# Kernel tuning notes

Hardware: AMD Instinct MI355X
Metric: run time of the kernel (lower is better)

## Reference

```python
import jax, jax.numpy as jnp
import numpy as np

N, E = 50000, 800000
CUR, HID, OUT = 128, 96, 128
NEG_SLOPE = 0.01  # F.leaky_relu default


def setup_inputs() -> dict:
    key = jax.random.key(0)
    ks = jax.random.split(key, 12)
    inv = lambda d: 1.0 / np.sqrt(d)
    return {
        "h": jax.random.normal(ks[0], (N, CUR), jnp.float32),
        "x": jax.random.normal(ks[1], (N, CUR), jnp.float32),
        "edge_index": jax.random.randint(ks[2], (2, E), 0, N, dtype=jnp.int64),
        "edge_weight": jax.random.uniform(ks[3], (E,), jnp.float32),
        # preprocessor_x: Linear(cur_dim, hidden_dim)
        "pre_W": jax.random.uniform(ks[4], (CUR, HID), jnp.float32, -inv(CUR), inv(CUR)),
        "pre_b": jax.random.uniform(ks[5], (HID,), jnp.float32, -inv(CUR), inv(CUR)),
        # SAGEConv(hidden, out): lin_l (neighbor, with bias) + lin_r (root, no bias)
        "sage_Wl": jax.random.uniform(ks[6], (HID, OUT), jnp.float32, -inv(HID), inv(HID)),
        "sage_bl": jnp.zeros((OUT,), jnp.float32),
        "sage_Wr": jax.random.uniform(ks[7], (HID, OUT), jnp.float32, -inv(HID), inv(HID)),
        # ARMAConv(hidden, out) with K=1 stacks, T=1 layers (PyG defaults)
        "arma_W": jax.random.uniform(ks[8], (HID, OUT), jnp.float32, -inv(HID), inv(HID)),
        "arma_V": jax.random.uniform(ks[9], (HID, OUT), jnp.float32, -inv(HID), inv(HID)),
        "arma_b": jnp.zeros((OUT,), jnp.float32),
    }


def _cell(x, src, dst, edge_weight, pre_W, pre_b,
          sage_Wl, sage_bl, sage_Wr, arma_W, arma_V, arma_b):
    n = x.shape[0]
    xh = x @ pre_W + pre_b  # [N, HID]

    # ---- SAGEConv: mean aggregation of edge-weighted neighbor features ----
    msg = xh[src] * edge_weight[:, None]                     # [E, HID]
    aggr = jax.ops.segment_sum(msg, dst, num_segments=n)     # [N, HID]
    cnt = jax.ops.segment_sum(jnp.ones_like(edge_weight), dst, num_segments=n)
    mean = aggr / jnp.maximum(cnt, 1.0)[:, None]
    o_sage = mean @ sage_Wl + sage_bl + xh @ sage_Wr         # [N, OUT]

    # ---- ARMAConv (K=1, T=1): ReLU(L_hat (x W) + x V + b) ----
    deg = jax.ops.segment_sum(edge_weight, dst, num_segments=n)
    dinv = jnp.where(deg > 0, jax.lax.rsqrt(jnp.maximum(deg, 1e-30)), 0.0)
    norm = dinv[src] * edge_weight * dinv[dst]               # [E]
    xw = xh @ arma_W                                         # [N, OUT]
    prop = jax.ops.segment_sum(xw[src] * norm[:, None], dst, num_segments=n)
    o_arma = jax.nn.relu(prop + xh @ arma_V + arma_b)        # [N, OUT]

    o1 = jax.nn.leaky_relu(o_sage, NEG_SLOPE)
    o2 = jax.nn.leaky_relu(o_arma, NEG_SLOPE)
    return jax.nn.relu(o1 + o2)


def reference(h, x, edge_index, edge_weight, pre_W, pre_b,
              sage_Wl, sage_bl, sage_Wr, arma_W, arma_V, arma_b):
    src, dst = edge_index[0], edge_index[1]
    his = x
    o3 = _cell(x, src, dst, edge_weight, pre_W, pre_b,
               sage_Wl, sage_bl, sage_Wr, arma_W, arma_V, arma_b)
    return (his, o3)
```

## Files before the change

kernel.cpp:

```cpp
#include <hip/hip_runtime.h>


typedef __attribute__((ext_vector_type(8))) short bf16x8;
typedef __attribute__((ext_vector_type(4))) float f32x4;

__device__ __forceinline__ float bf2f(unsigned short u) {
    return __uint_as_float(((unsigned)u) << 16);
}
__device__ __forceinline__ unsigned short f2bf(float f) {
    unsigned u = __float_as_uint(f);
    return (unsigned short)((u + 0x7FFFu + ((u >> 16) & 1u)) >> 16);
}

__device__ __forceinline__ int edge_src(const int* ei, int e, int E, int flag) {
    return flag ? ei[2 * e] : ei[e];
}
__device__ __forceinline__ int edge_dst(const int* ei, int e, int E, int flag) {
    return flag ? ei[2 * (E + e)] : ei[E + e];
}

__global__ void k_wprep(const unsigned* __restrict__ eiu,
                        const float* __restrict__ Wl, const float* __restrict__ Wr,
                        const float* __restrict__ Wa, const float* __restrict__ Va,
                        const float* __restrict__ preW,
                        unsigned short* __restrict__ Wf_s,
                        unsigned short* __restrict__ Wf_a,
                        unsigned short* __restrict__ Wfp,
                        int* __restrict__ flag,
                        int4* __restrict__ cnt4, int nz4) {
    if (blockIdx.x == 0) {
        __shared__ int bad;
        if (threadIdx.x == 0) bad = 0;
        __syncthreads();
        int nb = 0;
#pragma unroll
        for (int q = 0; q < 4; q++) {
            unsigned w = eiu[2 * (threadIdx.x * 4 + q) + 1];
            if (w != 0) nb++;
        }
        if (nb) atomicAdd(&bad, nb);
        __syncthreads();
        if (threadIdx.x == 0) *flag = (bad == 0) ? 1 : 0;
        return;
    }
    int tid = (blockIdx.x - 1) * blockDim.x + threadIdx.x;
    if (tid < 6144) {
        int mat = tid / 3072, rem = tid % 3072;
        int kstep = rem / 512, rem2 = rem % 512;
        int g = rem2 / 128, j = rem2 % 128;
        int k0 = kstep * 32 + g * 8;
        const float* Wtop = mat ? Wa : Wl;
        const float* Wbot = mat ? Va : Wr;
        unsigned short* dst = (mat ? Wf_a : Wf_s) + (((size_t)(kstep * 4 + g) * 128 + j) * 8);
#pragma unroll
        for (int kk = 0; kk < 8; kk++) {
            int k = k0 + kk;
            float v = (k < 96) ? Wtop[k * 128 + j] : Wbot[(k - 96) * 128 + j];
            dst[kk] = f2bf(v);
        }
    } else if (tid < 7680) {
        int rem = tid - 6144;
        int kstep = rem / 384, rem2 = rem % 384;
        int g = rem2 / 96, j = rem2 % 96;
        int k0 = kstep * 32 + g * 8;
        unsigned short* dst = Wfp + (((size_t)(kstep * 4 + g) * 96 + j) * 8);
#pragma unroll
        for (int kk = 0; kk < 8; kk++) dst[kk] = f2bf(preW[(k0 + kk) * 96 + j]);
    } else if (tid >= 8192 && tid < 8192 + nz4) {
        cnt4[tid - 8192] = make_int4(0, 0, 0, 0);
    }
}

__global__ __launch_bounds__(256) void k_xh_count(
    const float* __restrict__ x, const unsigned short* __restrict__ Wfp,
    const float* __restrict__ b, unsigned short* __restrict__ xhbf,
    float* __restrict__ out0, int N, int xhBlocks,
    const int* __restrict__ ei, int* __restrict__ cntS, int* __restrict__ pos,
    int E, const int* __restrict__ flagp) {
    __shared__ unsigned short X[64][136];
    if (blockIdx.x >= xhBlocks) {
        int e = (blockIdx.x - xhBlocks) * 256 + threadIdx.x;
        if (e < E) {
            int flag = *flagp;
            int d = edge_dst(ei, e, E, flag);
            int shard = blockIdx.x & 7;
            int lp = atomicAdd(&cntS[(size_t)shard * N + d], 1);
            pos[e] = (lp << 3) | shard;
        }
        return;
    }
    int t = threadIdx.x;
    int nb = blockIdx.x * 64;
    for (int u = t; u < 2048; u += 256) {
        int row = u >> 5, q = u & 31;
        long gn = nb + row;
        float4 v = make_float4(0.f, 0.f, 0.f, 0.f);
        if (gn < N) {
            v = ((const float4*)(x + gn * 128))[q];
            ((float4*)(out0 + gn * 128))[q] = v;
        }
        unsigned short* p = &X[row][q * 4];
        p[0] = f2bf(v.x); p[1] = f2bf(v.y); p[2] = f2bf(v.z); p[3] = f2bf(v.w);
    }
    __syncthreads();
    int lane = t & 63, w = t >> 6;
    int lr = lane & 15, lg = lane >> 4;
    bf16x8 a[4];
#pragma unroll
    for (int ks = 0; ks < 4; ks++)
        a[ks] = *(const bf16x8*)&X[w * 16 + lr][ks * 32 + lg * 8];
    for (int jt = 0; jt < 6; jt++) {
        f32x4 acc = {0.f, 0.f, 0.f, 0.f};
#pragma unroll
        for (int ks = 0; ks < 4; ks++) {
            bf16x8 bf = *(const bf16x8*)(Wfp + (((size_t)(ks * 4 + lg) * 96 + jt * 16 + lr) * 8));
            acc = __builtin_amdgcn_mfma_f32_16x16x32_bf16(a[ks], bf, acc, 0, 0, 0);
        }
        int h = jt * 16 + lr;
        float bb = b[h];
#pragma unroll
        for (int r = 0; r < 4; r++) {
            long n = nb + w * 16 + lg * 4 + r;
            if (n < N) xhbf[n * 96 + h] = f2bf(acc[r] + bb);
        }
    }
}

__global__ void k_scan_blk(const int* __restrict__ cntS, int* __restrict__ sdelta,
                           int* __restrict__ offs, int* __restrict__ bsum, int N) {
    __shared__ int sh[256];
    int t = threadIdx.x;
    int n = blockIdx.x * 256 + t;
    int total = 0;
    if (n < N) {
        int run = 0;
#pragma unroll
        for (int s = 0; s < 8; s++) {
            sdelta[(size_t)s * N + n] = run;
            run += cntS[(size_t)s * N + n];
        }
        total = run;
    }
    sh[t] = total;
    __syncthreads();
    for (int off = 1; off < 256; off <<= 1) {
        int add = (t >= off) ? sh[t - off] : 0;
        __syncthreads();
        sh[t] += add;
        __syncthreads();
    }
    if (n < N) offs[n + 1] = sh[t];
    if (t == 255) bsum[blockIdx.x] = sh[255];
    if (blockIdx.x == 0 && t == 0) offs[0] = 0;
}

__global__ void k_scan_top(int* __restrict__ bsum, int nb) {
    __shared__ int sh[256];
    int t = threadIdx.x;
    sh[t] = (t < nb) ? bsum[t] : 0;
    __syncthreads();
    for (int off = 1; off < 256; off <<= 1) {
        int add = (t >= off) ? sh[t - off] : 0;
        __syncthreads();
        sh[t] += add;
        __syncthreads();
    }
    bsum[t] = sh[t];
}

__global__ void k_scan_add(int* __restrict__ offs, const int* __restrict__ bsum, int N) {
    int t = threadIdx.x;
    int n = blockIdx.x * 256 + t;
    if (n < N && blockIdx.x > 0) offs[n + 1] += bsum[blockIdx.x - 1];
}

__global__ void k_fill(const int* __restrict__ ei, const float* __restrict__ ew,
                       const int* __restrict__ offs, const int* __restrict__ sdelta,
                       const int* __restrict__ pos, int* __restrict__ esrc,
                       float* __restrict__ eww, int E, int N,
                       const int* __restrict__ flagp) {
    int e = blockIdx.x * blockDim.x + threadIdx.x;
    if (e >= E) return;
    int flag = *flagp;
    int s = edge_src(ei, e, E, flag);
    int d = edge_dst(ei, e, E, flag);
    int pp = pos[e];
    int shard = pp & 7, lp = pp >> 3;
    int idx = offs[d] + sdelta[(size_t)shard * N + d] + lp;
    esrc[idx] = s;
    eww[idx] = ew[e];
}

__global__ void k_degcsr(const float* __restrict__ eww, const int* __restrict__ offs,
                         float* __restrict__ dinv, float* __restrict__ minv, int N) {
    int n = blockIdx.x * blockDim.x + threadIdx.x;
    if (n >= N) return;
    int beg = offs[n], end = offs[n + 1];
    float dg = 0.f;
    for (int e = beg; e < end; e++) dg += eww[e];
    dinv[n] = dg > 0.f ? rsqrtf(fmaxf(dg, 1e-30f)) : 0.f;
    minv[n] = 1.f / fmaxf((float)(end - beg), 1.f);
}

__global__ __launch_bounds__(256) void k_gather(
    const int* __restrict__ esrc, const float* __restrict__ eww,
    const unsigned short* __restrict__ xhbf, const int* __restrict__ offs,
    const float* __restrict__ dinv, const float* __restrict__ minv,
    unsigned short* __restrict__ meanbf, unsigned short* __restrict__ propbf, int N) {
    int lane = threadIdx.x & 63;
    int d = __builtin_amdgcn_readfirstlane(blockIdx.x * 4 + (threadIdx.x >> 6));
    if (d >= N) return;
    int beg = offs[d], end = offs[d + 1];
    bool act = lane < 48;
    int col = 2 * lane;
    float s0 = 0.f, s1 = 0.f, a0 = 0.f, a1 = 0.f;
    int e = beg;
    for (; e + 8 <= end; e += 8) {
        int idx[8]; float wgt[8], dv[8]; unsigned v[8];
#pragma unroll
        for (int q = 0; q < 8; q++) { idx[q] = esrc[e + q]; wgt[q] = eww[e + q]; }
#pragma unroll
        for (int q = 0; q < 8; q++) dv[q] = dinv[idx[q]];
#pragma unroll
        for (int q = 0; q < 8; q++)
            v[q] = act ? *(const unsigned*)(xhbf + (size_t)idx[q] * 96 + col) : 0u;
#pragma unroll
        for (int q = 0; q < 8; q++) {
            float x0 = bf2f((unsigned short)(v[q] & 0xffff));
            float x1 = bf2f((unsigned short)(v[q] >> 16));
            float w2 = wgt[q], dw = dv[q] * w2;
            s0 += w2 * x0; s1 += w2 * x1;
            a0 += dw * x0; a1 += dw * x1;
        }
    }
    for (; e + 4 <= end; e += 4) {
        int idx[4]; float wgt[4], dv[4]; unsigned v[4];
#pragma unroll
        for (int q = 0; q < 4; q++) { idx[q] = esrc[e + q]; wgt[q] = eww[e + q]; }
#pragma unroll
        for (int q = 0; q < 4; q++) dv[q] = dinv[idx[q]];
#pragma unroll
        for (int q = 0; q < 4; q++)
            v[q] = act ? *(const unsigned*)(xhbf + (size_t)idx[q] * 96 + col) : 0u;
#pragma unroll
        for (int q = 0; q < 4; q++) {
            float x0 = bf2f((unsigned short)(v[q] & 0xffff));
            float x1 = bf2f((unsigned short)(v[q] >> 16));
            float w2 = wgt[q], dw = dv[q] * w2;
            s0 += w2 * x0; s1 += w2 * x1;
            a0 += dw * x0; a1 += dw * x1;
        }
    }
    for (; e < end; e++) {
        int s = esrc[e];
        float w2 = eww[e];
        float ds = dinv[s];
        if (act) {
            unsigned v = *(const unsigned*)(xhbf + (size_t)s * 96 + col);
            float x0 = bf2f((unsigned short)(v & 0xffff));
            float x1 = bf2f((unsigned short)(v >> 16));
            s0 += w2 * x0; s1 += w2 * x1;
            a0 += ds * w2 * x0; a1 += ds * w2 * x1;
        }
    }
    if (act) {
        float mi = minv[d], di = dinv[d];
        unsigned mo = (unsigned)f2bf(s0 * mi) | ((unsigned)f2bf(s1 * mi) << 16);
        unsigned po = (unsigned)f2bf(a0 * di) | ((unsigned)f2bf(a1 * di) << 16);
        *(unsigned*)(meanbf + (size_t)d * 96 + col) = mo;
        *(unsigned*)(propbf + (size_t)d * 96 + col) = po;
    }
}

__global__ __launch_bounds__(256) void k_out(
    const unsigned short* __restrict__ meanbf, const unsigned short* __restrict__ propbf,
    const unsigned short* __restrict__ xhbf, const unsigned short* __restrict__ Wf_s,
    const unsigned short* __restrict__ Wf_a, const float* __restrict__ bl,
    const float* __restrict__ ba, float* __restrict__ out, int N) {
    __shared__ unsigned short A[3][64][104];
    int t = threadIdx.x;
    int nb = blockIdx.x * 64;
    for (int u = t; u < 2304; u += 256) {
        int arr = u / 768, rem = u - arr * 768;
        int row = rem / 12, c = rem - row * 12;
        long gn = nb + row;
        const unsigned short* src = (arr == 0) ? meanbf : (arr == 1) ? propbf : xhbf;
        float4 v = (gn < N) ? *(const float4*)(src + gn * 96 + c * 8)
                            : make_float4(0.f, 0.f, 0.f, 0.f);
        *(float4*)&A[arr][row][c * 8] = v;
    }
    __syncthreads();
    int lane = t & 63, w = t >> 6;
    int lr = lane & 15, lg = lane >> 4;
    bf16x8 am[3], ap[3], ax[3];
#pragma unroll
    for (int ks = 0; ks < 3; ks++) {
        int row = w * 16 + lr, kc = ks * 32 + lg * 8;
        am[ks] = *(const bf16x8*)&A[0][row][kc];
        ap[ks] = *(const bf16x8*)&A[1][row][kc];
        ax[ks] = *(const bf16x8*)&A[2][row][kc];
    }
    for (int jt = 0; jt < 8; jt++) {
        f32x4 accS = {0.f, 0.f, 0.f, 0.f};
        f32x4 accA = {0.f, 0.f, 0.f, 0.f};
#pragma unroll
        for (int ks = 0; ks < 3; ks++) {
            size_t boffS = ((size_t)(ks * 4 + lg) * 128 + jt * 16 + lr) * 8;
            size_t boffS2 = ((size_t)((ks + 3) * 4 + lg) * 128 + jt * 16 + lr) * 8;
            bf16x8 b0 = *(const bf16x8*)(Wf_s + boffS);
            bf16x8 b1 = *(const bf16x8*)(Wf_s + boffS2);
            bf16x8 b2 = *(const bf16x8*)(Wf_a + boffS);
            bf16x8 b3 = *(const bf16x8*)(Wf_a + boffS2);
            accS = __builtin_amdgcn_mfma_f32_16x16x32_bf16(am[ks], b0, accS, 0, 0, 0);
            accS = __builtin_amdgcn_mfma_f32_16x16x32_bf16(ax[ks], b1, accS, 0, 0, 0);
            accA = __builtin_amdgcn_mfma_f32_16x16x32_bf16(ap[ks], b2, accA, 0, 0, 0);
            accA = __builtin_amdgcn_mfma_f32_16x16x32_bf16(ax[ks], b3, accA, 0, 0, 0);
        }
        int j = jt * 16 + lr;
        float blj = bl[j], baj = ba[j];
#pragma unroll
        for (int r = 0; r < 4; r++) {
            long n = nb + w * 16 + lg * 4 + r;
            if (n < N) {
                float os = accS[r] + blj;
                float oa = fmaxf(accA[r] + baj, 0.f);
                float o1 = os > 0.f ? os : 0.01f * os;
                float o2 = oa > 0.f ? oa : 0.01f * oa;
                out[n * 128 + j] = fmaxf(o1 + o2, 0.f);
            }
        }
    }
}

extern "C" void kernel_launch(void* const* d_in, const int* in_sizes, int n_in,
                              void* d_out, int out_size, void* d_ws, size_t ws_size,
                              hipStream_t stream) {
    const float* x    = (const float*)d_in[1];
    const int*   ei   = (const int*)d_in[2];
    const float* ew   = (const float*)d_in[3];
    const float* preW = (const float*)d_in[4];
    const float* preb = (const float*)d_in[5];
    const float* Wl   = (const float*)d_in[6];
    const float* bl   = (const float*)d_in[7];
    const float* Wr   = (const float*)d_in[8];
    const float* Wa   = (const float*)d_in[9];
    const float* Va   = (const float*)d_in[10];
    const float* ba   = (const float*)d_in[11];

    const int N = in_sizes[1] / 128;
    const int E = in_sizes[3];
    const int NB = (N + 255) / 256;

    char* w = (char*)d_ws;
    unsigned short* xhbf   = (unsigned short*)w; w += (size_t)N * 96 * 2;
    unsigned short* meanbf = (unsigned short*)w; w += (size_t)N * 96 * 2;
    unsigned short* propbf = (unsigned short*)w; w += (size_t)N * 96 * 2;
    unsigned short* Wf_s   = (unsigned short*)w; w += (size_t)6 * 4 * 128 * 8 * 2;
    unsigned short* Wf_a   = (unsigned short*)w; w += (size_t)6 * 4 * 128 * 8 * 2;
    unsigned short* Wfp    = (unsigned short*)w; w += (size_t)4 * 4 * 96 * 8 * 2;
    int*   esrc   = (int*)w;   w += (size_t)E * 4;
    float* eww    = (float*)w; w += (size_t)E * 4;
    int*   pos    = (int*)w;   w += (size_t)E * 4;
    int*   cntS   = (int*)w;   w += (size_t)8 * N * 4;
    int*   sdelta = (int*)w;   w += (size_t)8 * N * 4;
    float* dinv   = (float*)w; w += (size_t)N * 4;
    float* minv   = (float*)w; w += (size_t)N * 4;
    int*   offs   = (int*)w;   w += (size_t)(N + 1) * 4;
    int*   bsum   = (int*)w;   w += 256 * 4;
    int*   flag   = (int*)w;

    const int nz4 = (8 * N + 3) / 4;
    const int wprep_blocks = 1 + (8192 + nz4 + 255) / 256;
    const int xhBlocks = (N + 63) / 64;
    const int cntBlocks = (E + 255) / 256;

    k_wprep<<<wprep_blocks, 256, 0, stream>>>((const unsigned*)ei, Wl, Wr, Wa, Va,
                                              preW, Wf_s, Wf_a, Wfp, flag,
                                              (int4*)cntS, nz4);
    k_xh_count<<<xhBlocks + cntBlocks, 256, 0, stream>>>(
        x, Wfp, preb, xhbf, (float*)d_out, N, xhBlocks, ei, cntS, pos, E, flag);
    k_scan_blk<<<NB, 256, 0, stream>>>(cntS, sdelta, offs, bsum, N);
    k_scan_top<<<1, 256, 0, stream>>>(bsum, NB);
    k_scan_add<<<NB, 256, 0, stream>>>(offs, bsum, N);
    k_fill<<<(E + 255) / 256, 256, 0, stream>>>(ei, ew, offs, sdelta, pos, esrc,
                                                eww, E, N, flag);
    k_degcsr<<<NB, 256, 0, stream>>>(eww, offs, dinv, minv, N);
    k_gather<<<(N + 3) / 4, 256, 0, stream>>>(esrc, eww, xhbf, offs, dinv,
                                              minv, meanbf, propbf, N);
    k_out<<<(N + 63) / 64, 256, 0, stream>>>(meanbf, propbf, xhbf, Wf_s, Wf_a,
                                             bl, ba, (float*)d_out + (size_t)N * 128, N);
}
```

Before: 147.5 us.

## Fuse scan, fill and degree kernels into one persistent kernel with grid barriers

Merges the three-stage block scan, CSR fill and degree computation into a single kernel of NB (~196) blocks, separated by software grid barriers built on atomic counters placed right after cntS so the existing zeroing covers them. This removes four kernel launches and their inter-kernel gaps. The cost is spin-wait barriers, which depend on all blocks being co-resident, and a fill phase that now runs on far fewer threads (each block loops over a slice of edges).

```diff
diff --git a/kernel.cpp b/kernel.cpp
--- a/kernel.cpp
+++ b/kernel.cpp
@@ -17,6 +17,17 @@
 }
 __device__ __forceinline__ int edge_dst(const int* ei, int e, int E, int flag) {
     return flag ? ei[2 * (E + e)] : ei[E + e];
+}
+
+__device__ __forceinline__ void gbar(int* ctr, int nb) {
+    __syncthreads();
+    if (threadIdx.x == 0) {
+        __threadfence();
+        atomicAdd(ctr, 1);
+        while (__hip_atomic_load(ctr, __ATOMIC_RELAXED, __HIP_MEMORY_SCOPE_AGENT) < nb) {}
+    }
+    __syncthreads();
+    __threadfence();
 }
 
 __global__ void k_wprep(const unsigned* __restrict__ eiu,
@@ -126,10 +137,16 @@
     }
 }
 
-__global__ void k_scan_blk(const int* __restrict__ cntS, int* __restrict__ sdelta,
-                           int* __restrict__ offs, int* __restrict__ bsum, int N) {
+__global__ __launch_bounds__(256) void k_mid(
+    const int* __restrict__ ei, const float* __restrict__ ew,
+    int* __restrict__ cntS, int* __restrict__ sdelta, int* __restrict__ offs,
+    int* __restrict__ bsum, int* __restrict__ bars,
+    const int* __restrict__ pos, int* __restrict__ esrc, float* __restrict__ eww,
+    float* __restrict__ dinv, float* __restrict__ minv,
+    int E, int N, int eperblk, const int* __restrict__ flagp) {
     __shared__ int sh[256];
     int t = threadIdx.x;
+    int nb_ = gridDim.x;
     int n = blockIdx.x * 256 + t;
     int total = 0;
     if (n < N) {
@@ -149,57 +166,41 @@
         sh[t] += add;
         __syncthreads();
     }
-    if (n < N) offs[n + 1] = sh[t];
+    int local_incl = sh[t];
     if (t == 255) bsum[blockIdx.x] = sh[255];
     if (blockIdx.x == 0 && t == 0) offs[0] = 0;
-}
-
-__global__ void k_scan_top(int* __restrict__ bsum, int nb) {
-    __shared__ int sh[256];
-    int t = threadIdx.x;
-    sh[t] = (t < nb) ? bsum[t] : 0;
-    __syncthreads();
-    for (int off = 1; off < 256; off <<= 1) {
-        int add = (t >= off) ? sh[t - off] : 0;
-        __syncthreads();
-        sh[t] += add;
-        __syncthreads();
-    }
-    bsum[t] = sh[t];
-}
-
-__global__ void k_scan_add(int* __restrict__ offs, const int* __restrict__ bsum, int N) {
-    int t = threadIdx.x;
-    int n = blockIdx.x * 256 + t;
-    if (n < N && blockIdx.x > 0) offs[n + 1] += bsum[blockIdx.x - 1];
-}
-
-__global__ void k_fill(const int* __restrict__ ei, const float* __restrict__ ew,
-                       const int* __restrict__ offs, const int* __restrict__ sdelta,
-                       const int* __restrict__ pos, int* __restrict__ esrc,
-                       float* __restrict__ eww, int E, int N,
-                       const int* __restrict__ flagp) {
-    int e = blockIdx.x * blockDim.x + threadIdx.x;
-    if (e >= E) return;
-    int flag = *flagp;
-    int s = edge_src(ei, e, E, flag);
-    int d = edge_dst(ei, e, E, flag);
-    int pp = pos[e];
-    int shard = pp & 7, lp = pp >> 3;
-    int idx = offs[d] + sdelta[(size_t)shard * N + d] + lp;
-    esrc[idx] = s;
-    eww[idx] = ew[e];
-}
-
-__global__ void k_degcsr(const float* __restrict__ eww, const int* __restrict__ offs,
-                         float* __restrict__ dinv, float* __restrict__ minv, int N) {
-    int n = blockIdx.x * blockDim.x + threadIdx.x;
-    if (n >= N) return;
-    int beg = offs[n], end = offs[n + 1];
-    float dg = 0.f;
-    for (int e = beg; e < end; e++) dg += eww[e];
-    dinv[n] = dg > 0.f ? rsqrtf(fmaxf(dg, 1e-30f)) : 0.f;
-    minv[n] = 1.f / fmaxf((float)(end - beg), 1.f);
+    gbar(&bars[0], nb_);
+    sh[t] = (t < blockIdx.x) ? bsum[t] : 0;
+    __syncthreads();
+    for (int s = 128; s > 0; s >>= 1) {
+        if (t < s) sh[t] += sh[t + s];
+        __syncthreads();
+    }
+    int base = sh[0];
+    if (n < N) offs[n + 1] = base + local_incl;
+    gbar(&bars[1], nb_);
+    {
+        int flag = *flagp;
+        int e0 = blockIdx.x * eperblk;
+        int e1 = min(e0 + eperblk, E);
+        for (int e = e0 + t; e < e1; e += 256) {
+            int s = edge_src(ei, e, E, flag);
+            int d = edge_dst(ei, e, E, flag);
+            int pp = pos[e];
+            int shard = pp & 7, lp = pp >> 3;
+            int idx = offs[d] + sdelta[(size_t)shard * N + d] + lp;
+            esrc[idx] = s;
+            eww[idx] = ew[e];
+        }
+    }
+    gbar(&bars[2], nb_);
+    if (n < N) {
+        int beg = offs[n], end = offs[n + 1];
+        float dg = 0.f;
+        for (int e = beg; e < end; e++) dg += eww[e];
+        dinv[n] = dg > 0.f ? rsqrtf(fmaxf(dg, 1e-30f)) : 0.f;
+        minv[n] = 1.f / fmaxf((float)(end - beg), 1.f);
+    }
 }
 
 __global__ __launch_bounds__(256) void k_gather(
@@ -362,6 +363,7 @@
     float* eww    = (float*)w; w += (size_t)E * 4;
     int*   pos    = (int*)w;   w += (size_t)E * 4;
     int*   cntS   = (int*)w;   w += (size_t)8 * N * 4;
+    int*   bars   = (int*)w;   w += 4 * 4;
     int*   sdelta = (int*)w;   w += (size_t)8 * N * 4;
     float* dinv   = (float*)w; w += (size_t)N * 4;
     float* minv   = (float*)w; w += (size_t)N * 4;
@@ -369,22 +371,19 @@
     int*   bsum   = (int*)w;   w += 256 * 4;
     int*   flag   = (int*)w;
 
-    const int nz4 = (8 * N + 3) / 4;
+    const int nz4 = (8 * N + 4 + 3) / 4;
     const int wprep_blocks = 1 + (8192 + nz4 + 255) / 256;
     const int xhBlocks = (N + 63) / 64;
     const int cntBlocks = (E + 255) / 256;
+    const int eperblk = (E + NB - 1) / NB;
 
     k_wprep<<<wprep_blocks, 256, 0, stream>>>((const unsigned*)ei, Wl, Wr, Wa, Va,
                                               preW, Wf_s, Wf_a, Wfp, flag,
                                               (int4*)cntS, nz4);
     k_xh_count<<<xhBlocks + cntBlocks, 256, 0, stream>>>(
         x, Wfp, preb, xhbf, (float*)d_out, N, xhBlocks, ei, cntS, pos, E, flag);
-    k_scan_blk<<<NB, 256, 0, stream>>>(cntS, sdelta, offs, bsum, N);
-    k_scan_top<<<1, 256, 0, stream>>>(bsum, NB);
-    k_scan_add<<<NB, 256, 0, stream>>>(offs, bsum, N);
-    k_fill<<<(E + 255) / 256, 256, 0, stream>>>(ei, ew, offs, sdelta, pos, esrc,
-                                                eww, E, N, flag);
-    k_degcsr<<<NB, 256, 0, stream>>>(eww, offs, dinv, minv, N);
+    k_mid<<<NB, 256, 0, stream>>>(ei, ew, cntS, sdelta, offs, bsum, bars, pos,
+                                  esrc, eww, dinv, minv, E, N, eperblk, flag);
     k_gather<<<(N + 3) / 4, 256, 0, stream>>>(esrc, eww, xhbf, offs, dinv,
                                               minv, meanbf, propbf, N);
     k_out<<<(N + 63) / 64, 256, 0, stream>>>(meanbf, propbf, xhbf, Wf_s, Wf_a,
```

Result: slower. 215.7 us (+46.2%).
